# Optimization experiments

Hardware: AMD Instinct MI355X
Metric: run time of the kernel (lower is better)

The kernel has to match this reference:

```python
import jax, jax.numpy as jnp
import numpy as np

N_SRC, N_DST, N_EDGES = 50000, 50000, 500000
IN_DIM, OUT_DIM, EDGE_DIM = 128, 128, 11
BN_EPS = 1e-5


def setup_inputs() -> dict:
    key = jax.random.key(0)
    ks = jax.random.split(key, 16)
    s = 0.05
    return {
        "src_feat": jax.random.normal(ks[0], (N_SRC, IN_DIM), jnp.float32),
        "dst_feat": jax.random.normal(ks[1], (N_DST, IN_DIM), jnp.float32),
        "edge_feats": jax.random.normal(ks[2], (N_EDGES, EDGE_DIM), jnp.float32),
        "src_idx": jax.random.randint(ks[3], (N_EDGES,), 0, N_SRC, jnp.int32),
        "dst_idx": jax.random.randint(ks[4], (N_EDGES,), 0, N_DST, jnp.int32),
        "W_src": jax.random.normal(ks[5], (IN_DIM, OUT_DIM), jnp.float32) * s,
        "b_src": jnp.zeros((OUT_DIM,), jnp.float32),
        "W_dst": jax.random.normal(ks[6], (IN_DIM, OUT_DIM), jnp.float32) * s,
        "b_dst": jnp.zeros((OUT_DIM,), jnp.float32),
        "W_edge": jax.random.normal(ks[7], (EDGE_DIM, OUT_DIM), jnp.float32) * s,
        "b_edge": jnp.zeros((OUT_DIM,), jnp.float32),
        "attn_w": jax.random.normal(ks[8], (3 * OUT_DIM,), jnp.float32) * s,
        "attn_b": jnp.zeros((), jnp.float32),
        "gamma": jnp.ones((OUT_DIM,), jnp.float32),
        "beta": jnp.zeros((OUT_DIM,), jnp.float32),
        "alpha": jnp.asarray(0.25, jnp.float32),
    }


def reference(src_feat, dst_feat, edge_feats, src_idx, dst_idx,
              W_src, b_src, W_dst, b_dst, W_edge, b_edge,
              attn_w, attn_b, gamma, beta, alpha):
    D = W_src.shape[1]
    # project at node/edge level (math identical to projecting gathered feats)
    hs = src_feat @ W_src + b_src            # [Ns, D]  (linear_src)
    hd = dst_feat @ W_dst + b_dst            # [Nd, D]  (linear_dst)
    ep = edge_feats @ W_edge + b_edge        # [E, D]   (linear_edge)
    # attn_l on concat([src, dst, edge]) == sum of three dot products + bias
    aw_s, aw_d, aw_e = attn_w[:D], attn_w[D:2 * D], attn_w[2 * D:]
    a = (hs @ aw_s)[src_idx] + (hd @ aw_d)[dst_idx] + ep @ aw_e + attn_b  # [E]
    # edge softmax over incoming edges of each dst node
    n_dst = dst_feat.shape[0]
    seg_max = jax.ops.segment_max(a, dst_idx, num_segments=n_dst)
    a_exp = jnp.exp(a - seg_max[dst_idx])
    denom = jax.ops.segment_sum(a_exp, dst_idx, num_segments=n_dst)
    attn = a_exp / denom[dst_idx]            # [E]
    # weighted message = attn * linear_src(src_h); scatter-sum to dst
    msg = attn[:, None] * hs[src_idx]        # [E, D]
    h_new = jax.ops.segment_sum(msg, dst_idx, num_segments=n_dst)  # [Nd, D]
    # BatchNorm1d (training-mode batch statistics)
    mean = jnp.mean(h_new, axis=0)
    var = jnp.var(h_new, axis=0)
    h_bn = (h_new - mean) / jnp.sqrt(var + BN_EPS) * gamma + beta
    # PReLU (single shared alpha); dropout is identity in eval
    return jnp.where(h_bn >= 0, h_bn, alpha * h_bn)
```

## Files before the change

kernel.cpp:

```cpp
#include <hip/hip_runtime.h>
#include <cstddef>

#define NSRC 50000
#define NDST 50000
#define NEDGE 500000
#define DIM 128
#define EDIM 11
#define BN_EPS 1e-5f
#define SCAN_NBLK ((NDST + 255) / 256)

#define HS_BLOCKS ((NSRC + 63) / 64)
#define DS_BLOCKS ((NDST + 31) / 32)
#define ED_BLOCKS ((NEDGE + 1023) / 1024)

#define OFF_HS      0
#define OFF_SSCORE  (OFF_HS + (size_t)NSRC*DIM)
#define OFF_DSCORE  (OFF_SSCORE + NSRC)
#define OFF_EE      (OFF_DSCORE + NDST)
#define OFF_DEG     (OFF_EE + NEDGE)
#define OFF_COLSUM  (OFF_DEG + NDST)
#define OFF_COLSQ   (OFF_COLSUM + 128)
#define OFF_OFFS    (OFF_COLSQ + 128)
#define OFF_CURSOR  (OFF_OFFS + NDST + 2)
#define OFF_PAIRS   (OFF_CURSOR + NDST)
#define OFF_WDVEC   (OFF_PAIRS + 2*(size_t)NEDGE)
#define OFF_WEVEC   (OFF_WDVEC + 128)
#define OFF_SCAL    (OFF_WEVEC + 16)
#define OFF_PART    (OFF_SCAL + 4)

__global__ void k_prep(const float* __restrict__ W_dst, const float* __restrict__ b_dst,
                       const float* __restrict__ W_edge, const float* __restrict__ b_edge,
                       const float* __restrict__ attn_w, const float* __restrict__ attn_b,
                       float* __restrict__ wd_vec, float* __restrict__ we_vec,
                       float* __restrict__ scal) {
    int t = threadIdx.x;
    float acc = 0.f;
    for (int d = 0; d < DIM; ++d) acc += W_dst[t * DIM + d] * attn_w[DIM + d];
    wd_vec[t] = acc;
    if (t < EDIM) {
        float e = 0.f;
        for (int d = 0; d < DIM; ++d) e += W_edge[t * DIM + d] * attn_w[2 * DIM + d];
        we_vec[t] = e;
    }
    __shared__ float red[128];
    red[t] = b_dst[t] * attn_w[DIM + t];
    __syncthreads();
    for (int s = 64; s > 0; s >>= 1) { if (t < s) red[t] += red[t + s]; __syncthreads(); }
    if (t == 0) scal[0] = red[0];
    __syncthreads();
    red[t] = b_edge[t] * attn_w[2 * DIM + t];
    __syncthreads();
    for (int s = 64; s > 0; s >>= 1) { if (t < s) red[t] += red[t + s]; __syncthreads(); }
    if (t == 0) scal[1] = red[0] + attn_b[0];
}

__global__ __launch_bounds__(256) void k_fused(const float* __restrict__ A,
                                               const float* __restrict__ W,
                                               const float* __restrict__ bias,
                                               const float* __restrict__ attn_w,
                                               const float* __restrict__ B,
                                               const float* __restrict__ ef,
                                               const int* __restrict__ dst_idx,
                                               const float* __restrict__ wd_vec,
                                               const float* __restrict__ we_vec,
                                               const float* __restrict__ scal,
                                               float* __restrict__ hs,
                                               float* __restrict__ s_score,
                                               float* __restrict__ d_score,
                                               float* __restrict__ ee,
                                               int* __restrict__ deg) {
    __shared__ float Ws[32][128];
    __shared__ float As[64][36];
    const int bid = blockIdx.x;
    const int t = threadIdx.x;

    if (bid < HS_BLOCKS) {
        const int r0 = bid * 64;
        const int tc = t & 15;
        const int tr4 = (t >> 4) * 4;
        const int c0 = tc * 8;
        float acc[4][8];
        #pragma unroll
        for (int i = 0; i < 4; ++i)
            #pragma unroll
            for (int j = 0; j < 8; ++j) acc[i][j] = 0.f;

        for (int k0 = 0; k0 < DIM; k0 += 32) {
            #pragma unroll
            for (int i = 0; i < 4; ++i) {
                int f = t + 256 * i;
                int row = f >> 5, c4 = f & 31;
                float4 v = *reinterpret_cast<const float4*>(W + (size_t)(k0 + row) * DIM + c4 * 4);
                *reinterpret_cast<float4*>(&Ws[row][c4 * 4]) = v;
            }
            #pragma unroll
            for (int i = 0; i < 2; ++i) {
                int f = t + 256 * i;
                int row = f >> 3, c4 = f & 7;
                int gr = r0 + row;
                float4 v = make_float4(0.f, 0.f, 0.f, 0.f);
                if (gr < NSRC) v = *reinterpret_cast<const float4*>(A + (size_t)gr * DIM + k0 + c4 * 4);
                *reinterpret_cast<float4*>(&As[row][c4 * 4]) = v;
            }
            __syncthreads();

            #pragma unroll 4
            for (int kk = 0; kk < 32; ++kk) {
                float a0 = As[tr4 + 0][kk];
                float a1 = As[tr4 + 1][kk];
                float a2 = As[tr4 + 2][kk];
                float a3 = As[tr4 + 3][kk];
                float4 w0 = *reinterpret_cast<const float4*>(&Ws[kk][c0]);
                float4 w1 = *reinterpret_cast<const float4*>(&Ws[kk][c0 + 4]);
                acc[0][0] += a0 * w0.x; acc[0][1] += a0 * w0.y; acc[0][2] += a0 * w0.z; acc[0][3] += a0 * w0.w;
                acc[0][4] += a0 * w1.x; acc[0][5] += a0 * w1.y; acc[0][6] += a0 * w1.z; acc[0][7] += a0 * w1.w;
                acc[1][0] += a1 * w0.x; acc[1][1] += a1 * w0.y; acc[1][2] += a1 * w0.z; acc[1][3] += a1 * w0.w;
                acc[1][4] += a1 * w1.x; acc[1][5] += a1 * w1.y; acc[1][6] += a1 * w1.z; acc[1][7] += a1 * w1.w;
                acc[2][0] += a2 * w0.x; acc[2][1] += a2 * w0.y; acc[2][2] += a2 * w0.z; acc[2][3] += a2 * w0.w;
                acc[2][4] += a2 * w1.x; acc[2][5] += a2 * w1.y; acc[2][6] += a2 * w1.z; acc[2][7] += a2 * w1.w;
                acc[3][0] += a3 * w0.x; acc[3][1] += a3 * w0.y; acc[3][2] += a3 * w0.z; acc[3][3] += a3 * w0.w;
                acc[3][4] += a3 * w1.x; acc[3][5] += a3 * w1.y; acc[3][6] += a3 * w1.z; acc[3][7] += a3 * w1.w;
            }
            __syncthreads();
        }

        float4 b0 = *reinterpret_cast<const float4*>(bias + c0);
        float4 b1 = *reinterpret_cast<const float4*>(bias + c0 + 4);
        float4 aw0 = *reinterpret_cast<const float4*>(attn_w + c0);
        float4 aw1 = *reinterpret_cast<const float4*>(attn_w + c0 + 4);
        #pragma unroll
        for (int i = 0; i < 4; ++i) {
            int gr = r0 + tr4 + i;
            acc[i][0] += b0.x; acc[i][1] += b0.y; acc[i][2] += b0.z; acc[i][3] += b0.w;
            acc[i][4] += b1.x; acc[i][5] += b1.y; acc[i][6] += b1.z; acc[i][7] += b1.w;
            float p = acc[i][0] * aw0.x + acc[i][1] * aw0.y + acc[i][2] * aw0.z + acc[i][3] * aw0.w
                    + acc[i][4] * aw1.x + acc[i][5] * aw1.y + acc[i][6] * aw1.z + acc[i][7] * aw1.w;
            p += __shfl_xor(p, 1);
            p += __shfl_xor(p, 2);
            p += __shfl_xor(p, 4);
            p += __shfl_xor(p, 8);
            if (gr < NSRC) {
                float4* o = reinterpret_cast<float4*>(hs + (size_t)gr * DIM + c0);
                o[0] = make_float4(acc[i][0], acc[i][1], acc[i][2], acc[i][3]);
                o[1] = make_float4(acc[i][4], acc[i][5], acc[i][6], acc[i][7]);
                if (tc == 0) s_score[gr] = p;
            }
        }
    } else if (bid < HS_BLOCKS + DS_BLOCKS) {
        int row = (bid - HS_BLOCKS) * 32 + (t >> 3);
        int c0 = (t & 7) * 16;
        if (row >= NDST) return;
        const float4* x = reinterpret_cast<const float4*>(B + (size_t)row * DIM + c0);
        const float4* w = reinterpret_cast<const float4*>(wd_vec + c0);
        float p = 0.f;
        #pragma unroll
        for (int i = 0; i < 4; ++i) {
            float4 a = x[i], b = w[i];
            p += a.x * b.x + a.y * b.y + a.z * b.z + a.w * b.w;
        }
        p += __shfl_xor(p, 1);
        p += __shfl_xor(p, 2);
        p += __shfl_xor(p, 4);
        if ((t & 7) == 0) d_score[row] = p + scal[0];
    } else {
        float wv[EDIM];
        #pragma unroll
        for (int k = 0; k < EDIM; ++k) wv[k] = we_vec[k];
        float s1 = scal[1];
        int ebase = (bid - HS_BLOCKS - DS_BLOCKS) * 1024 + t;
        #pragma unroll
        for (int i = 0; i < 4; ++i) {
            int e = ebase + i * 256;
            if (e < NEDGE) {
                const float* er = ef + (size_t)e * EDIM;
                float a = s1;
                #pragma unroll
                for (int k = 0; k < EDIM; ++k) a += er[k] * wv[k];
                ee[e] = a;
                atomicAdd(&deg[dst_idx[e]], 1);
            }
        }
    }
}

__global__ __launch_bounds__(256) void k_scanA(const int* __restrict__ deg,
                                               int* __restrict__ off,
                                               int* __restrict__ partials) {
    __shared__ int tmp[256];
    int t = threadIdx.x;
    int i = blockIdx.x * 256 + t;
    int v = (i < NDST) ? deg[i] : 0;
    tmp[t] = v;
    __syncthreads();
    #pragma unroll
    for (int d = 1; d < 256; d <<= 1) {
        int u = (t >= d) ? tmp[t - d] : 0;
        __syncthreads();
        tmp[t] += u;
        __syncthreads();
    }
    if (i < NDST) off[i] = tmp[t] - v;
    if (t == 255) partials[blockIdx.x] = tmp[255];
}

__global__ __launch_bounds__(256) void k_scanB(int* __restrict__ partials) {
    __shared__ int tmp[256];
    int t = threadIdx.x;
    int v = (t < SCAN_NBLK) ? partials[t] : 0;
    tmp[t] = v;
    __syncthreads();
    #pragma unroll
    for (int d = 1; d < 256; d <<= 1) {
        int u = (t >= d) ? tmp[t - d] : 0;
        __syncthreads();
        tmp[t] += u;
        __syncthreads();
    }
    if (t < SCAN_NBLK) partials[t] = tmp[t] - v;
}

__global__ __launch_bounds__(256) void k_scanC(int* __restrict__ off,
                                               int* __restrict__ cursor,
                                               const int* __restrict__ partials) {
    int t = threadIdx.x;
    int i = blockIdx.x * 256 + t;
    if (i < NDST) {
        int f = off[i] + partials[blockIdx.x];
        off[i] = f;
        cursor[i] = f;
    }
    if (i == 0) off[NDST] = NEDGE;
}

__global__ __launch_bounds__(256) void k_scat(const int* __restrict__ src_idx,
                                              const int* __restrict__ dst_idx,
                                              const float* __restrict__ ee,
                                              const float* __restrict__ s_score,
                                              const float* __restrict__ d_score,
                                              int* __restrict__ cursor,
                                              int2* __restrict__ pairs) {
    int base = blockIdx.x * 1024 + threadIdx.x;
    #pragma unroll
    for (int i = 0; i < 4; ++i) {
        int e = base + i * 256;
        if (e < NEDGE) {
            int s = src_idx[e], d = dst_idx[e];
            float w = expf(ee[e] + s_score[s] + d_score[d]);
            int pos = atomicAdd(&cursor[d], 1);
            pairs[pos] = make_int2(s, __float_as_int(w));
        }
    }
}

__global__ __launch_bounds__(256) void k_gather(const float* __restrict__ hs,
                                                const int* __restrict__ off,
                                                const int2* __restrict__ pairs,
                                                float* __restrict__ h_new) {
    int wid = (blockIdx.x * blockDim.x + threadIdx.x) >> 6;
    int lane = threadIdx.x & 63;
    if (wid >= NDST) return;
    int b = off[wid], e2 = off[wid + 1];
    int deg = e2 - b;
    float ax = 0.f, ay = 0.f, wsum = 0.f;

    for (int base = 0; base < deg; base += 64) {
        int cnt = min(deg - base, 64);
        int myS = 0;
        float myW = 0.f;
        if (lane < cnt) {
            int2 p = pairs[b + base + lane];
            myS = p.x;
            myW = __int_as_float(p.y);
        }
        wsum += myW;

        int j = 0;
        for (; j + 4 <= cnt; j += 4) {
            int s0 = __shfl(myS, j + 0), s1 = __shfl(myS, j + 1);
            int s2 = __shfl(myS, j + 2), s3 = __shfl(myS, j + 3);
            float w0 = __shfl(myW, j + 0), w1 = __shfl(myW, j + 1);
            float w2 = __shfl(myW, j + 2), w3 = __shfl(myW, j + 3);
            float2 v0 = reinterpret_cast<const float2*>(hs + (size_t)s0 * DIM)[lane];
            float2 v1 = reinterpret_cast<const float2*>(hs + (size_t)s1 * DIM)[lane];
            float2 v2 = reinterpret_cast<const float2*>(hs + (size_t)s2 * DIM)[lane];
            float2 v3 = reinterpret_cast<const float2*>(hs + (size_t)s3 * DIM)[lane];
            ax += w0 * v0.x + w1 * v1.x + w2 * v2.x + w3 * v3.x;
            ay += w0 * v0.y + w1 * v1.y + w2 * v2.y + w3 * v3.y;
        }
        for (; j < cnt; ++j) {
            int s0 = __shfl(myS, j);
            float w0 = __shfl(myW, j);
            float2 v0 = reinterpret_cast<const float2*>(hs + (size_t)s0 * DIM)[lane];
            ax += w0 * v0.x;
            ay += w0 * v0.y;
        }
    }

    #pragma unroll
    for (int m = 1; m < 64; m <<= 1) wsum += __shfl_xor(wsum, m);

    float inv = (deg > 0) ? 1.f / wsum : 0.f;
    reinterpret_cast<float2*>(h_new + (size_t)wid * DIM)[lane] = make_float2(ax * inv, ay * inv);
}

__global__ __launch_bounds__(256) void k_bnstats(const float* __restrict__ h,
                                                 float* __restrict__ colsum,
                                                 float* __restrict__ colsq) {
    int col = threadIdx.x & 127;
    int rp = threadIdx.x >> 7;
    float s = 0.f, q = 0.f;
    for (int r = blockIdx.x * 2 + rp; r < NDST; r += gridDim.x * 2) {
        float x = h[(size_t)r * DIM + col];
        s += x;
        q += x * x;
    }
    __shared__ float ls[2][128], lq[2][128];
    ls[rp][col] = s;
    lq[rp][col] = q;
    __syncthreads();
    if (rp == 0) {
        atomicAdd(&colsum[col], ls[0][col] + ls[1][col]);
        atomicAdd(&colsq[col], lq[0][col] + lq[1][col]);
    }
}

__global__ __launch_bounds__(256) void k_bnfinal(float* __restrict__ h,
                                                 const float* __restrict__ colsum,
                                                 const float* __restrict__ colsq,
                                                 const float* __restrict__ gamma,
                                                 const float* __restrict__ beta,
                                                 const float* __restrict__ alpha_p) {
    const size_t total4 = (size_t)NDST * DIM / 4;
    const float alpha = alpha_p[0];
    const float invN = 1.f / (float)NDST;
    const int c0 = (threadIdx.x & 31) * 4;
    float sc[4], sh[4];
    #pragma unroll
    for (int k = 0; k < 4; ++k) {
        float mean = colsum[c0 + k] * invN;
        float var = colsq[c0 + k] * invN - mean * mean;
        float s = gamma[c0 + k] * rsqrtf(var + BN_EPS);
        sc[k] = s;
        sh[k] = beta[c0 + k] - mean * s;
    }
    size_t stride = (size_t)gridDim.x * blockDim.x;
    for (size_t i = blockIdx.x * blockDim.x + threadIdx.x; i < total4; i += stride) {
        float4 x = reinterpret_cast<float4*>(h)[i];
        float y0 = x.x * sc[0] + sh[0];
        float y1 = x.y * sc[1] + sh[1];
        float y2 = x.z * sc[2] + sh[2];
        float y3 = x.w * sc[3] + sh[3];
        float4 o;
        o.x = y0 >= 0.f ? y0 : alpha * y0;
        o.y = y1 >= 0.f ? y1 : alpha * y1;
        o.z = y2 >= 0.f ? y2 : alpha * y2;
        o.w = y3 >= 0.f ? y3 : alpha * y3;
        reinterpret_cast<float4*>(h)[i] = o;
    }
}

extern "C" void kernel_launch(void* const* d_in, const int* in_sizes, int n_in,
                              void* d_out, int out_size, void* d_ws, size_t ws_size,
                              hipStream_t stream) {
    const float* src_feat   = (const float*)d_in[0];
    const float* dst_feat   = (const float*)d_in[1];
    const float* edge_feats = (const float*)d_in[2];
    const int*   src_idx    = (const int*)d_in[3];
    const int*   dst_idx    = (const int*)d_in[4];
    const float* W_src      = (const float*)d_in[5];
    const float* b_src      = (const float*)d_in[6];
    const float* W_dst      = (const float*)d_in[7];
    const float* b_dst      = (const float*)d_in[8];
    const float* W_edge     = (const float*)d_in[9];
    const float* b_edge     = (const float*)d_in[10];
    const float* attn_w     = (const float*)d_in[11];
    const float* attn_b     = (const float*)d_in[12];
    const float* gamma      = (const float*)d_in[13];
    const float* beta       = (const float*)d_in[14];
    const float* alpha      = (const float*)d_in[15];

    float* ws      = (float*)d_ws;
    float* hs      = ws + OFF_HS;
    float* s_score = ws + OFF_SSCORE;
    float* d_score = ws + OFF_DSCORE;
    float* ee      = ws + OFF_EE;
    int*   deg     = (int*)(ws + OFF_DEG);
    float* colsum  = ws + OFF_COLSUM;
    float* colsq   = ws + OFF_COLSQ;
    int*   off     = (int*)(ws + OFF_OFFS);
    int*   cursor  = (int*)(ws + OFF_CURSOR);
    int2*  pairs   = (int2*)(ws + OFF_PAIRS);
    float* wd_vec  = ws + OFF_WDVEC;
    float* we_vec  = ws + OFF_WEVEC;
    float* scal    = ws + OFF_SCAL;
    int*   part    = (int*)(ws + OFF_PART);

    float* h_new = (float*)d_out;

    hipMemsetAsync(deg, 0, (NDST + 256) * sizeof(float), stream);

    k_prep<<<1, 128, 0, stream>>>(W_dst, b_dst, W_edge, b_edge, attn_w, attn_b,
                                  wd_vec, we_vec, scal);
    k_fused<<<HS_BLOCKS + DS_BLOCKS + ED_BLOCKS, 256, 0, stream>>>(
        src_feat, W_src, b_src, attn_w, dst_feat, edge_feats, dst_idx,
        wd_vec, we_vec, scal, hs, s_score, d_score, ee, deg);
    k_scanA<<<SCAN_NBLK, 256, 0, stream>>>(deg, off, part);
    k_scanB<<<1, 256, 0, stream>>>(part);
    k_scanC<<<SCAN_NBLK, 256, 0, stream>>>(off, cursor, part);
    k_scat<<<ED_BLOCKS, 256, 0, stream>>>(src_idx, dst_idx, ee, s_score, d_score,
                                          cursor, pairs);
    k_gather<<<(NDST * 64 + 255) / 256, 256, 0, stream>>>(hs, off, pairs, h_new);
    k_bnstats<<<512, 256, 0, stream>>>(h_new, colsum, colsq);
    k_bnfinal<<<1024, 256, 0, stream>>>(h_new, colsum, colsq, gamma, beta, alpha);
}
```

Baseline: 166.1 us.

## Compute src projection with bf16 MFMA using pre-transposed bf16 weights

```diff
diff --git a/kernel.cpp b/kernel.cpp
--- a/kernel.cpp
+++ b/kernel.cpp
@@ -12,6 +12,9 @@
 #define HS_BLOCKS ((NSRC + 63) / 64)
 #define DS_BLOCKS ((NDST + 31) / 32)
 #define ED_BLOCKS ((NEDGE + 1023) / 1024)
+
+typedef short bf16x8 __attribute__((ext_vector_type(8)));
+typedef float f32x4 __attribute__((ext_vector_type(4)));
 
 #define OFF_HS      0
 #define OFF_SSCORE  (OFF_HS + (size_t)NSRC*DIM)
@@ -27,6 +30,13 @@
 #define OFF_WEVEC   (OFF_WDVEC + 128)
 #define OFF_SCAL    (OFF_WEVEC + 16)
 #define OFF_PART    (OFF_SCAL + 4)
+#define OFF_WT      (((OFF_PART + 256 + 3) / 4) * 4)
+
+__device__ __forceinline__ unsigned short f2bf(float x) {
+    unsigned int u = __float_as_uint(x);
+    u += 0x7FFFu + ((u >> 16) & 1u);
+    return (unsigned short)(u >> 16);
+}
 
 __global__ void k_prep(const float* __restrict__ W_dst, const float* __restrict__ b_dst,
                        const float* __restrict__ W_edge, const float* __restrict__ b_edge,
@@ -54,8 +64,29 @@
     if (t == 0) scal[1] = red[0] + attn_b[0];
 }
 
+__global__ __launch_bounds__(256) void k_wt(const float* __restrict__ W,
+                                            unsigned short* __restrict__ wt) {
+    __shared__ float tile[32][33];
+    int bi = blockIdx.x & 3;
+    int bj = blockIdx.x >> 2;
+    int t = threadIdx.x;
+    int cl = t & 31;
+    #pragma unroll
+    for (int i = 0; i < 4; ++i) {
+        int kl = (t >> 5) * 4 + i;
+        tile[kl][cl] = W[(size_t)(bi * 32 + kl) * DIM + bj * 32 + cl];
+    }
+    __syncthreads();
+    int ko = t & 31;
+    #pragma unroll
+    for (int i = 0; i < 4; ++i) {
+        int co = (t >> 5) * 4 + i;
+        wt[(size_t)(bj * 32 + co) * DIM + bi * 32 + ko] = f2bf(tile[ko][co]);
+    }
+}
+
 __global__ __launch_bounds__(256) void k_fused(const float* __restrict__ A,
-                                               const float* __restrict__ W,
+                                               const unsigned short* __restrict__ wt,
                                                const float* __restrict__ bias,
                                                const float* __restrict__ attn_w,
                                                const float* __restrict__ B,
@@ -69,81 +100,76 @@
                                                float* __restrict__ d_score,
                                                float* __restrict__ ee,
                                                int* __restrict__ deg) {
-    __shared__ float Ws[32][128];
-    __shared__ float As[64][36];
     const int bid = blockIdx.x;
     const int t = threadIdx.x;
 
     if (bid < HS_BLOCKS) {
-        const int r0 = bid * 64;
-        const int tc = t & 15;
-        const int tr4 = (t >> 4) * 4;
-        const int c0 = tc * 8;
-        float acc[4][8];
-        #pragma unroll
-        for (int i = 0; i < 4; ++i)
+        const int wv = t >> 6;
+        const int lane = t & 63;
+        const int lrow = lane & 15;
+        const int kg = lane >> 4;
+        const int grow = bid * 64 + wv * 16 + lrow;
+        const bool rowok = grow < NSRC;
+        const float* arow = A + (size_t)grow * DIM;
+
+        bf16x8 af[4];
+        #pragma unroll
+        for (int s = 0; s < 4; ++s) {
+            float4 p0 = make_float4(0.f, 0.f, 0.f, 0.f), p1 = p0;
+            if (rowok) {
+                p0 = *reinterpret_cast<const float4*>(arow + 32 * s + kg * 8);
+                p1 = *reinterpret_cast<const float4*>(arow + 32 * s + kg * 8 + 4);
+            }
+            bf16x8 a;
+            a[0] = (short)f2bf(p0.x); a[1] = (short)f2bf(p0.y);
+            a[2] = (short)f2bf(p0.z); a[3] = (short)f2bf(p0.w);
+            a[4] = (short)f2bf(p1.x); a[5] = (short)f2bf(p1.y);
+            a[6] = (short)f2bf(p1.z); a[7] = (short)f2bf(p1.w);
+            af[s] = a;
+        }
+
+        f32x4 acc[8];
+        #pragma unroll
+        for (int c = 0; c < 8; ++c) acc[c] = (f32x4){0.f, 0.f, 0.f, 0.f};
+
+        #pragma unroll
+        for (int c = 0; c < 8; ++c) {
             #pragma unroll
-            for (int j = 0; j < 8; ++j) acc[i][j] = 0.f;
-
-        for (int k0 = 0; k0 < DIM; k0 += 32) {
+            for (int s = 0; s < 4; ++s) {
+                const bf16x8 b = *reinterpret_cast<const bf16x8*>(
+                    wt + ((size_t)(16 * c + lrow) * DIM + 32 * s + kg * 8));
+                acc[c] = __builtin_amdgcn_mfma_f32_16x16x32_bf16(af[s], b, acc[c], 0, 0, 0);
+            }
+        }
+
+        float p[4] = {0.f, 0.f, 0.f, 0.f};
+        #pragma unroll
+        for (int c = 0; c < 8; ++c) {
+            float bb = bias[16 * c + lrow];
+            float aw = attn_w[16 * c + lrow];
             #pragma unroll
             for (int i = 0; i < 4; ++i) {
-                int f = t + 256 * i;
-                int row = f >> 5, c4 = f & 31;
-                float4 v = *reinterpret_cast<const float4*>(W + (size_t)(k0 + row) * DIM + c4 * 4);
-                *reinterpret_cast<float4*>(&Ws[row][c4 * 4]) = v;
+                float v = acc[c][i] + bb;
+                acc[c][i] = v;
+                p[i] += v * aw;
             }
-            #pragma unroll
-            for (int i = 0; i < 2; ++i) {
-                int f = t + 256 * i;
-                int row = f >> 3, c4 = f & 7;
-                int gr = r0 + row;
-                float4 v = make_float4(0.f, 0.f, 0.f, 0.f);
-                if (gr < NSRC) v = *reinterpret_cast<const float4*>(A + (size_t)gr * DIM + k0 + c4 * 4);
-                *reinterpret_cast<float4*>(&As[row][c4 * 4]) = v;
-            }
-            __syncthreads();
-
-            #pragma unroll 4
-            for (int kk = 0; kk < 32; ++kk) {
-                float a0 = As[tr4 + 0][kk];
-                float a1 = As[tr4 + 1][kk];
-                float a2 = As[tr4 + 2][kk];
-                float a3 = As[tr4 + 3][kk];
-                float4 w0 = *reinterpret_cast<const float4*>(&Ws[kk][c0]);
-                float4 w1 = *reinterpret_cast<const float4*>(&Ws[kk][c0 + 4]);
-                acc[0][0] += a0 * w0.x; acc[0][1] += a0 * w0.y; acc[0][2] += a0 * w0.z; acc[0][3] += a0 * w0.w;
-                acc[0][4] += a0 * w1.x; acc[0][5] += a0 * w1.y; acc[0][6] += a0 * w1.z; acc[0][7] += a0 * w1.w;
-                acc[1][0] += a1 * w0.x; acc[1][1] += a1 * w0.y; acc[1][2] += a1 * w0.z; acc[1][3] += a1 * w0.w;
-                acc[1][4] += a1 * w1.x; acc[1][5] += a1 * w1.y; acc[1][6] += a1 * w1.z; acc[1][7] += a1 * w1.w;
-                acc[2][0] += a2 * w0.x; acc[2][1] += a2 * w0.y; acc[2][2] += a2 * w0.z; acc[2][3] += a2 * w0.w;
-                acc[2][4] += a2 * w1.x; acc[2][5] += a2 * w1.y; acc[2][6] += a2 * w1.z; acc[2][7] += a2 * w1.w;
-                acc[3][0] += a3 * w0.x; acc[3][1] += a3 * w0.y; acc[3][2] += a3 * w0.z; acc[3][3] += a3 * w0.w;
-                acc[3][4] += a3 * w1.x; acc[3][5] += a3 * w1.y; acc[3][6] += a3 * w1.z; acc[3][7] += a3 * w1.w;
-            }
-            __syncthreads();
-        }
-
-        float4 b0 = *reinterpret_cast<const float4*>(bias + c0);
-        float4 b1 = *reinterpret_cast<const float4*>(bias + c0 + 4);
-        float4 aw0 = *reinterpret_cast<const float4*>(attn_w + c0);
-        float4 aw1 = *reinterpret_cast<const float4*>(attn_w + c0 + 4);
+        }
         #pragma unroll
         for (int i = 0; i < 4; ++i) {
-            int gr = r0 + tr4 + i;
-            acc[i][0] += b0.x; acc[i][1] += b0.y; acc[i][2] += b0.z; acc[i][3] += b0.w;
-            acc[i][4] += b1.x; acc[i][5] += b1.y; acc[i][6] += b1.z; acc[i][7] += b1.w;
-            float p = acc[i][0] * aw0.x + acc[i][1] * aw0.y + acc[i][2] * aw0.z + acc[i][3] * aw0.w
-                    + acc[i][4] * aw1.x + acc[i][5] * aw1.y + acc[i][6] * aw1.z + acc[i][7] * aw1.w;
-            p += __shfl_xor(p, 1);
-            p += __shfl_xor(p, 2);
-            p += __shfl_xor(p, 4);
-            p += __shfl_xor(p, 8);
-            if (gr < NSRC) {
-                float4* o = reinterpret_cast<float4*>(hs + (size_t)gr * DIM + c0);
-                o[0] = make_float4(acc[i][0], acc[i][1], acc[i][2], acc[i][3]);
-                o[1] = make_float4(acc[i][4], acc[i][5], acc[i][6], acc[i][7]);
-                if (tc == 0) s_score[gr] = p;
+            p[i] += __shfl_xor(p[i], 1);
+            p[i] += __shfl_xor(p[i], 2);
+            p[i] += __shfl_xor(p[i], 4);
+            p[i] += __shfl_xor(p[i], 8);
+        }
+        const int orow0 = bid * 64 + wv * 16 + kg * 4;
+        #pragma unroll
+        for (int i = 0; i < 4; ++i) {
+            int orow = orow0 + i;
+            if (orow < NSRC) {
+                #pragma unroll
+                for (int c = 0; c < 8; ++c)
+                    hs[(size_t)orow * DIM + 16 * c + lrow] = acc[c][i];
+                if (lrow == 0) s_score[orow] = p[i];
             }
         }
     } else if (bid < HS_BLOCKS + DS_BLOCKS) {
@@ -394,6 +420,7 @@
     float* we_vec  = ws + OFF_WEVEC;
     float* scal    = ws + OFF_SCAL;
     int*   part    = (int*)(ws + OFF_PART);
+    unsigned short* wt = (unsigned short*)(ws + OFF_WT);
 
     float* h_new = (float*)d_out;
 
@@ -401,8 +428,9 @@
 
     k_prep<<<1, 128, 0, stream>>>(W_dst, b_dst, W_edge, b_edge, attn_w, attn_b,
                                   wd_vec, we_vec, scal);
+    k_wt<<<16, 256, 0, stream>>>(W_src, wt);
     k_fused<<<HS_BLOCKS + DS_BLOCKS + ED_BLOCKS, 256, 0, stream>>>(
-        src_feat, W_src, b_src, attn_w, dst_feat, edge_feats, dst_idx,
+        src_feat, wt, b_src, attn_w, dst_feat, edge_feats, dst_idx,
         wd_vec, we_vec, scal, hs, s_score, d_score, ee, deg);
     k_scanA<<<SCAN_NBLK, 256, 0, stream>>>(deg, off, part);
     k_scanB<<<1, 256, 0, stream>>>(part);
```

Result: slower. 171.2 us (+3.1%).
